# Optimization experiments

Hardware: AMD Instinct MI355X
Metric: run time of the kernel (lower is better)

Reference implementation:

```python
import jax, jax.numpy as jnp
import numpy as np

V, E, H = 32000, 512, 512
B, T = 4, 2048


def setup_inputs() -> dict:
    key = jax.random.key(0)
    ks = jax.random.split(key, 10)
    s_e = 1.0 / np.sqrt(E)
    s_h = 1.0 / np.sqrt(H)
    emb = jax.random.normal(ks[0], (V, E), jnp.float32) * 0.02
    emb = emb.at[0].set(0.0)  # padding_idx=0
    return {
        "x": jax.random.randint(ks[1], (B, T), 0, V),
        "emb": emb,
        "W_ih": jax.random.uniform(ks[2], (3 * H, E), jnp.float32, -s_h, s_h),
        "W_hh": jax.random.uniform(ks[3], (3 * H, H), jnp.float32, -s_h, s_h),
        "b_ih": jnp.zeros((3 * H,), jnp.float32),
        "b_hh": jnp.zeros((3 * H,), jnp.float32),
        "Wq": jax.random.uniform(ks[4], (H, H), jnp.float32, -s_h, s_h),
        "bq": jnp.zeros((H,), jnp.float32),
        "Wk": jax.random.uniform(ks[5], (H, H), jnp.float32, -s_h, s_h),
        "bk": jnp.zeros((H,), jnp.float32),
        "Wv": jax.random.uniform(ks[6], (H, H), jnp.float32, -s_h, s_h),
        "bv": jnp.zeros((H,), jnp.float32),
        "Wfc": jax.random.uniform(ks[7], (V, H), jnp.float32, -s_h, s_h),
        "bfc": jnp.zeros((V,), jnp.float32),
    }


def _gru(z, W_ih, W_hh, b_ih, b_hh):
    # z: [B,T,E] -> hidden states [B,T,H]; PyTorch gate order r,z,n.
    b, t, _ = z.shape
    h_dim = W_hh.shape[1]
    xg = jnp.einsum('bte,ge->btg', z, W_ih) + b_ih  # [B,T,3H]

    def step(h, xt):
        gh = h @ W_hh.T + b_hh
        xr, xz, xn = jnp.split(xt, 3, axis=-1)
        hr, hz, hn = jnp.split(gh, 3, axis=-1)
        r = jax.nn.sigmoid(xr + hr)
        zg = jax.nn.sigmoid(xz + hz)
        n = jnp.tanh(xn + r * hn)
        h_new = (1.0 - zg) * n + zg * h
        return h_new, h_new

    h0 = jnp.zeros((b, h_dim), z.dtype)
    _, hs = jax.lax.scan(step, h0, jnp.swapaxes(xg, 0, 1))  # [T,B,H]
    return jnp.swapaxes(hs, 0, 1)


def reference(x, emb, W_ih, W_hh, b_ih, b_hh, Wq, bq, Wk, bk, Wv, bv, Wfc, bfc):
    z = emb[x]                                   # [B,T,E]
    h = _gru(z, W_ih, W_hh, b_ih, b_hh)          # [B,T,H]
    q = h @ Wq.T + bq
    k = h @ Wk.T + bk
    v = h @ Wv.T + bv
    hd = h.shape[-1]
    score = jnp.einsum('bqd,bkd->bqk', q, k) / jnp.sqrt(jnp.float32(hd))
    t = score.shape[-1]
    causal = jnp.triu(jnp.ones((t, t), bool), k=1)  # True above diagonal
    score = jnp.where(causal[None], jnp.float32(-1e9), score)
    attn = jax.nn.softmax(score, axis=-1)
    ctx = jnp.einsum('bqk,bkd->bqd', attn, v)
    return ctx @ Wfc.T + bfc                      # [B,T,V]
```

## Files before the change

### kernel.cpp

```cpp
#include <hip/hip_runtime.h>

#define Bn 4
#define Tn 2048
#define Hn 512
#define En 512
#define Vn 32000
#define G3 1536
#define BT (Bn*Tn)

typedef __bf16 bf16x8 __attribute__((ext_vector_type(8)));
typedef float f32x4 __attribute__((ext_vector_type(4)));

__device__ __forceinline__ unsigned short f2bf(float f) {
  unsigned int u = __float_as_uint(f);
  u += 0x7fffu + ((u >> 16) & 1u);
  return (unsigned short)(u >> 16);
}

__global__ __launch_bounds__(256) void cvt_bf16_kernel(const float* __restrict__ in,
                                                       unsigned short* __restrict__ outp) {
  size_t idx = (size_t)blockIdx.x * 256 + threadIdx.x;
  float4 f = *(const float4*)(in + idx * 4);
  uint2 o;
  o.x = (unsigned int)f2bf(f.x) | ((unsigned int)f2bf(f.y) << 16);
  o.y = (unsigned int)f2bf(f.z) | ((unsigned int)f2bf(f.w) << 16);
  *(uint2*)(outp + idx * 4) = o;
}

__global__ __launch_bounds__(256) void gather_emb_kernel(const int* __restrict__ x,
                                                         const float* __restrict__ emb,
                                                         unsigned short* __restrict__ embb) {
  size_t idx = ((size_t)blockIdx.x * 256 + threadIdx.x) * 8;
  int row = (int)(idx >> 9), e = (int)(idx & 511);
  const float* src = emb + (size_t)x[row] * En + e;
  float4 f0 = *(const float4*)(src);
  float4 f1 = *(const float4*)(src + 4);
  uint4 o;
  o.x = (unsigned)f2bf(f0.x) | ((unsigned)f2bf(f0.y) << 16);
  o.y = (unsigned)f2bf(f0.z) | ((unsigned)f2bf(f0.w) << 16);
  o.z = (unsigned)f2bf(f1.x) | ((unsigned)f2bf(f1.y) << 16);
  o.w = (unsigned)f2bf(f1.z) | ((unsigned)f2bf(f1.w) << 16);
  *(uint4*)(embb + idx) = o;
}

__global__ __launch_bounds__(256) void xg_mm_kernel(const unsigned short* __restrict__ A,
                                                    const unsigned short* __restrict__ Bw,
                                                    const float* __restrict__ bias,
                                                    float* __restrict__ out) {
  __shared__ unsigned short a_lds[128 * 40];
  __shared__ unsigned short b_lds[128 * 40];
  int n0 = blockIdx.x * 128, m0 = blockIdx.y * 128;
  int tid = threadIdx.x;
  int wid = tid >> 6, lane = tid & 63;
  int wm = wid >> 1, wn = wid & 1;
  f32x4 acc[4][4];
#pragma unroll
  for (int mf = 0; mf < 4; ++mf)
#pragma unroll
    for (int nf = 0; nf < 4; ++nf) {
      acc[mf][nf][0] = 0.0f; acc[mf][nf][1] = 0.0f;
      acc[mf][nf][2] = 0.0f; acc[mf][nf][3] = 0.0f;
    }
  int kcol = (lane >> 4) * 8;
  int rbase = lane & 15;
  for (int k0 = 0; k0 < 512; k0 += 32) {
#pragma unroll
    for (int sidx = 0; sidx < 2; ++sidx) {
      int slot = tid + sidx * 256;
      int row = slot >> 2, c8 = (slot & 3) * 8;
      uint4 av = *(const uint4*)(A  + (size_t)(m0 + row) * 512 + k0 + c8);
      *(uint4*)&a_lds[row * 40 + c8] = av;
      uint4 bv = *(const uint4*)(Bw + (size_t)(n0 + row) * 512 + k0 + c8);
      *(uint4*)&b_lds[row * 40 + c8] = bv;
    }
    __syncthreads();
    bf16x8 af[4], bf[4];
#pragma unroll
    for (int mf = 0; mf < 4; ++mf)
      af[mf] = *(const bf16x8*)&a_lds[(wm*64 + mf*16 + rbase) * 40 + kcol];
#pragma unroll
    for (int nf = 0; nf < 4; ++nf)
      bf[nf] = *(const bf16x8*)&b_lds[(wn*64 + nf*16 + rbase) * 40 + kcol];
#pragma unroll
    for (int mf = 0; mf < 4; ++mf)
#pragma unroll
      for (int nf = 0; nf < 4; ++nf)
        acc[mf][nf] = __builtin_amdgcn_mfma_f32_16x16x32_bf16(af[mf], bf[nf], acc[mf][nf], 0, 0, 0);
    __syncthreads();
  }
  int rgrp = (lane >> 4) * 4;
#pragma unroll
  for (int mf = 0; mf < 4; ++mf)
#pragma unroll
    for (int nf = 0; nf < 4; ++nf) {
      int col = n0 + wn*64 + nf*16 + (lane & 15);
      float bc = bias[col];
#pragma unroll
      for (int i2 = 0; i2 < 4; ++i2) {
        int row = m0 + wm*64 + mf*16 + rgrp + i2;
        out[(size_t)row * G3 + col] = acc[mf][nf][i2] + bc;
      }
    }
}

__global__ __launch_bounds__(256) void qkv_mm_kernel(const unsigned short* __restrict__ A,
                                                     const unsigned short* __restrict__ Bw,
                                                     const float* __restrict__ bq,
                                                     const float* __restrict__ bk,
                                                     const float* __restrict__ bv,
                                                     unsigned short* __restrict__ qb,
                                                     unsigned short* __restrict__ kb,
                                                     unsigned short* __restrict__ vb) {
  __shared__ unsigned short a_lds[128 * 40];
  __shared__ unsigned short b_lds[128 * 40];
  int n0 = blockIdx.x * 128, m0 = blockIdx.y * 128;
  int seg = n0 >> 9;
  const float* bias = (seg == 0) ? bq : (seg == 1) ? bk : bv;
  unsigned short* outp = (seg == 0) ? qb : (seg == 1) ? kb : vb;
  int nc0 = n0 & 511;
  int tid = threadIdx.x;
  int wid = tid >> 6, lane = tid & 63;
  int wm = wid >> 1, wn = wid & 1;
  f32x4 acc[4][4];
#pragma unroll
  for (int mf = 0; mf < 4; ++mf)
#pragma unroll
    for (int nf = 0; nf < 4; ++nf) {
      acc[mf][nf][0] = 0.0f; acc[mf][nf][1] = 0.0f;
      acc[mf][nf][2] = 0.0f; acc[mf][nf][3] = 0.0f;
    }
  int kcol = (lane >> 4) * 8;
  int rbase = lane & 15;
  for (int k0 = 0; k0 < 512; k0 += 32) {
#pragma unroll
    for (int sidx = 0; sidx < 2; ++sidx) {
      int slot = tid + sidx * 256;
      int row = slot >> 2, c8 = (slot & 3) * 8;
      uint4 av = *(const uint4*)(A  + (size_t)(m0 + row) * 512 + k0 + c8);
      *(uint4*)&a_lds[row * 40 + c8] = av;
      uint4 bv4 = *(const uint4*)(Bw + (size_t)(n0 + row) * 512 + k0 + c8);
      *(uint4*)&b_lds[row * 40 + c8] = bv4;
    }
    __syncthreads();
    bf16x8 af[4], bf[4];
#pragma unroll
    for (int mf = 0; mf < 4; ++mf)
      af[mf] = *(const bf16x8*)&a_lds[(wm*64 + mf*16 + rbase) * 40 + kcol];
#pragma unroll
    for (int nf = 0; nf < 4; ++nf)
      bf[nf] = *(const bf16x8*)&b_lds[(wn*64 + nf*16 + rbase) * 40 + kcol];
#pragma unroll
    for (int mf = 0; mf < 4; ++mf)
#pragma unroll
      for (int nf = 0; nf < 4; ++nf)
        acc[mf][nf] = __builtin_amdgcn_mfma_f32_16x16x32_bf16(af[mf], bf[nf], acc[mf][nf], 0, 0, 0);
    __syncthreads();
  }
  int rgrp = (lane >> 4) * 4;
#pragma unroll
  for (int mf = 0; mf < 4; ++mf)
#pragma unroll
    for (int nf = 0; nf < 4; ++nf) {
      int col = nc0 + wn*64 + nf*16 + (lane & 15);
      float bc = bias[col];
#pragma unroll
      for (int i2 = 0; i2 < 4; ++i2) {
        int row = m0 + wm*64 + mf*16 + rgrp + i2;
        outp[(size_t)row * Hn + col] = f2bf(acc[mf][nf][i2] + bc);
      }
    }
}

__global__ __launch_bounds__(256, 1) void gru_kernel(const float* __restrict__ Whh,
                                                     const float* __restrict__ bhh,
                                                     const float* __restrict__ xg,
                                                     unsigned short* __restrict__ hsb,
                                                     unsigned long long* __restrict__ th) {
  __shared__ float w_lds[6][512];
  int tid = threadIdx.x;
  int g = blockIdx.x;
  int jb = g * 2;
  int w = tid >> 6, lane = tid & 63;

  for (int d = 0; d < 6; ++d) {
    const float* wr = Whh + (size_t)((d >> 1) * 512 + jb + (d & 1)) * 512;
    int e0 = tid, e1 = tid + 256;
    int s0 = e0 >> 6, l0 = e0 & 63;
    int s1 = e1 >> 6, l1 = e1 & 63;
    w_lds[d][e0] = wr[(s0 >> 1) * 128 + 2 * l0 + (s0 & 1)];
    w_lds[d][e1] = wr[(s1 >> 1) * 128 + 2 * l1 + (s1 & 1)];
  }
  float bh_r = 0.0f, bh_z = 0.0f, bh_n = 0.0f;
  if (lane < 2) {
    bh_r = bhh[jb + lane];
    bh_z = bhh[512 + jb + lane];
    bh_n = bhh[1024 + jb + lane];
  }
  float hown = 0.0f;
  __syncthreads();

  const unsigned long long RDYM = 0x0000000100000001ULL;
  for (int t = 0; t < Tn; ++t) {
    float xr = 0.0f, xz = 0.0f, xn = 0.0f;
    if (lane < 2) {
      size_t xb = ((size_t)(w * Tn + t)) * G3 + jb + lane;
      xr = xg[xb]; xz = xg[xb + 512]; xn = xg[xb + 1024];
    }
    float hlo[4], hhi[4];
    if (t > 0) {
      const unsigned long long* tp = th + (size_t)(t - 1) * 1024 + w * 256;
      unsigned long long v[4];
      unsigned rdy = 0;
      do {
#pragma unroll
        for (int q = 0; q < 4; ++q)
          if (!(rdy & (1u << q)))
            v[q] = __hip_atomic_load(tp + q * 64 + lane, __ATOMIC_RELAXED,
                                     __HIP_MEMORY_SCOPE_AGENT);
#pragma unroll
        for (int q = 0; q < 4; ++q)
          if ((v[q] & RDYM) == RDYM) rdy |= 1u << q;
      } while (!__all(rdy == 15u));
#pragma unroll
      for (int q = 0; q < 4; ++q) {
        hlo[q] = __uint_as_float((unsigned)v[q]);
        hhi[q] = __uint_as_float((unsigned)(v[q] >> 32));
      }
    } else {
#pragma unroll
      for (int q = 0; q < 4; ++q) { hlo[q] = 0.0f; hhi[q] = 0.0f; }
    }

    float p[6];
#pragma unroll
    for (int d = 0; d < 6; ++d) {
      float s = w_lds[d][lane] * hlo[0];
      s = fmaf(w_lds[d][64 + lane], hhi[0], s);
#pragma unroll
      for (int q = 1; q < 4; ++q) {
        s = fmaf(w_lds[d][(2 * q) * 64 + lane], hlo[q], s);
        s = fmaf(w_lds[d][(2 * q + 1) * 64 + lane], hhi[q], s);
      }
      p[d] = s;
    }

    float mm[3];
#pragma unroll
    for (int j = 0; j < 3; ++j) {
      float a = p[2 * j], b = p[2 * j + 1];
      bool odd = (lane & 1);
      float send = odd ? a : b;
      float rx = __shfl_xor(send, 1);
      float m = (odd ? b : a) + rx;
      m += __shfl_xor(m, 2);
      m += __shfl_xor(m, 4);
      m += __shfl_xor(m, 8);
      m += __shfl_xor(m, 16);
      m += __shfl_xor(m, 32);
      mm[j] = m;
    }
    if (lane < 2) {
      float dr = mm[0], dz = mm[1], dn = mm[2];
      float rr = __builtin_amdgcn_rcpf(1.0f + __expf(-(xr + dr + bh_r)));
      float zz = __builtin_amdgcn_rcpf(1.0f + __expf(-(xz + dz + bh_z)));
      float ta = xn + rr * (dn + bh_n);
      float nn = 1.0f - 2.0f * __builtin_amdgcn_rcpf(__expf(2.0f * ta) + 1.0f);
      hown = (1.0f - zz) * nn + zz * hown;
    }
    unsigned myb = __float_as_uint(hown) | 1u;
    unsigned other = __shfl(myb, 1);
    if (lane == 0) {
      unsigned long long pk = ((unsigned long long)other << 32) | myb;
      __hip_atomic_store(th + (size_t)t * 1024 + w * 256 + g, pk,
                         __ATOMIC_RELAXED, __HIP_MEMORY_SCOPE_AGENT);
    }
    if (lane < 2)
      hsb[((size_t)w * Tn + t) * Hn + jb + lane] = f2bf(hown);
  }
}

__global__ __launch_bounds__(256) void vt_kernel(const unsigned short* __restrict__ v,
                                                 unsigned short* __restrict__ vT) {
  __shared__ unsigned short tl[64][80];
  int b = blockIdx.z;
  int t0 = blockIdx.x * 64, e0 = blockIdx.y * 64;
  int tid = threadIdx.x;
  int r = tid >> 2, c16 = (tid & 3) * 16;
  const unsigned short* src = v + (size_t)b * Tn * Hn + (size_t)(t0 + r) * Hn + e0 + c16;
  uint4 a0 = *(const uint4*)(src);
  uint4 a1 = *(const uint4*)(src + 8);
  *(uint4*)&tl[r][c16]     = a0;
  *(uint4*)&tl[r][c16 + 8] = a1;
  __syncthreads();
  unsigned short* dst = vT + (size_t)b * Hn * Tn + (size_t)(e0 + r) * Tn + t0 + c16;
  unsigned int o[8];
#pragma unroll
  for (int ii = 0; ii < 8; ++ii)
    o[ii] = (unsigned)tl[c16 + 2*ii][r] | ((unsigned)tl[c16 + 2*ii + 1][r] << 16);
  uint4 o0; o0.x = o[0]; o0.y = o[1]; o0.z = o[2]; o0.w = o[3];
  uint4 o1; o1.x = o[4]; o1.y = o[5]; o1.z = o[6]; o1.w = o[7];
  *(uint4*)(dst)     = o0;
  *(uint4*)(dst + 8) = o1;
}

__global__ __launch_bounds__(256) void score_kernel(const unsigned short* __restrict__ qb,
                                                    const unsigned short* __restrict__ kbp,
                                                    float* __restrict__ s) {
  if (blockIdx.x > blockIdx.y) return;
  __shared__ unsigned short a_lds[128 * 40];
  __shared__ unsigned short b_lds[128 * 40];
  int b = blockIdx.z;
  int n0 = blockIdx.x * 128, m0 = blockIdx.y * 128;
  const unsigned short* A  = qb  + (size_t)b * Tn * Hn;
  const unsigned short* Bw = kbp + (size_t)b * Tn * Hn;
  int tid = threadIdx.x;
  int wid = tid >> 6, lane = tid & 63;
  int wm = wid >> 1, wn = wid & 1;
  f32x4 acc[4][4];
#pragma unroll
  for (int mf = 0; mf < 4; ++mf)
#pragma unroll
    for (int nf = 0; nf < 4; ++nf) {
      acc[mf][nf][0] = 0.0f; acc[mf][nf][1] = 0.0f;
      acc[mf][nf][2] = 0.0f; acc[mf][nf][3] = 0.0f;
    }
  int kcol = (lane >> 4) * 8;
  int rbase = lane & 15;
  for (int k0 = 0; k0 < Hn; k0 += 32) {
#pragma unroll
    for (int sidx = 0; sidx < 2; ++sidx) {
      int slot = tid + sidx * 256;
      int row = slot >> 2, c8 = (slot & 3) * 8;
      uint4 av = *(const uint4*)(A  + (size_t)(m0 + row) * Hn + k0 + c8);
      *(uint4*)&a_lds[row * 40 + c8] = av;
      uint4 bv = *(const uint4*)(Bw + (size_t)(n0 + row) * Hn + k0 + c8);
      *(uint4*)&b_lds[row * 40 + c8] = bv;
    }
    __syncthreads();
    bf16x8 af[4], bf[4];
#pragma unroll
    for (int mf = 0; mf < 4; ++mf)
      af[mf] = *(const bf16x8*)&a_lds[(wm*64 + mf*16 + rbase) * 40 + kcol];
#pragma unroll
    for (int nf = 0; nf < 4; ++nf)
      bf[nf] = *(const bf16x8*)&b_lds[(wn*64 + nf*16 + rbase) * 40 + kcol];
#pragma unroll
    for (int mf = 0; mf < 4; ++mf)
#pragma unroll
      for (int nf = 0; nf < 4; ++nf)
        acc[mf][nf] = __builtin_amdgcn_mfma_f32_16x16x32_bf16(af[mf], bf[nf], acc[mf][nf], 0, 0, 0);
    __syncthreads();
  }
  const float scale = 0.04419417382415922f;
  int rgrp = (lane >> 4) * 4;
#pragma unroll
  for (int mf = 0; mf < 4; ++mf)
#pragma unroll
    for (int nf = 0; nf < 4; ++nf) {
      int col = n0 + wn*64 + nf*16 + (lane & 15);
#pragma unroll
      for (int i2 = 0; i2 < 4; ++i2) {
        int row = m0 + wm*64 + mf*16 + rgrp + i2;
        s[(size_t)b*Tn*Tn + (size_t)row*Tn + col] = acc[mf][nf][i2] * scale;
      }
    }
}

__global__ __launch_bounds__(256) void softmax_kernel(float* __restrict__ s,
                                                      unsigned short* __restrict__ ab) {
  int row = blockIdx.x;
  int b = row >> 11, i = row & 2047;
  float* p = s + (size_t)b*Tn*Tn + (size_t)i*Tn;
  unsigned short* a = ab + ((size_t)b*Tn + i) * Tn;
  int len = i + 1;
  int padEnd = ((i >> 7) + 1) << 7;
  int tid = threadIdx.x;
  __shared__ float redm[4];
  __shared__ float reds[4];
  float m = -1e30f;
  for (int j = tid; j < len; j += 256) m = fmaxf(m, p[j]);
#pragma unroll
  for (int off = 32; off > 0; off >>= 1) m = fmaxf(m, __shfl_down(m, off));
  if ((tid & 63) == 0) redm[tid >> 6] = m;
  __syncthreads();
  if (tid == 0) redm[0] = fmaxf(fmaxf(redm[0], redm[1]), fmaxf(redm[2], redm[3]));
  __syncthreads();
  m = redm[0];
  float sum = 0.0f;
  for (int j = tid; j < len; j += 256) {
    float e = __expf(p[j] - m);
    p[j] = e;
    sum += e;
  }
#pragma unroll
  for (int off = 32; off > 0; off >>= 1) sum += __shfl_down(sum, off);
  if ((tid & 63) == 0) reds[tid >> 6] = sum;
  __syncthreads();
  if (tid == 0) reds[0] = reds[0] + reds[1] + reds[2] + reds[3];
  __syncthreads();
  float inv = 1.0f / reds[0];
  for (int j = tid; j < len; j += 256) a[j] = f2bf(p[j] * inv);
  for (int j = len + tid; j < padEnd; j += 256) a[j] = 0;
}

__global__ __launch_bounds__(256) void ctx_kernel(const unsigned short* __restrict__ ab,
                                                  const unsigned short* __restrict__ vT,
                                                  unsigned short* __restrict__ ctxb) {
  __shared__ unsigned short a_lds[128 * 40];
  __shared__ unsigned short b_lds[128 * 40];
  int b = blockIdx.z;
  int n0 = blockIdx.x * 128, m0 = blockIdx.y * 128;
  int kmax = (blockIdx.y + 1) * 128;
  const unsigned short* A  = ab + (size_t)b * Tn * Tn;
  const unsigned short* Bw = vT + (size_t)b * Hn * Tn;
  int tid = threadIdx.x;
  int wid = tid >> 6, lane = tid & 63;
  int wm = wid >> 1, wn = wid & 1;
  f32x4 acc[4][4];
#pragma unroll
  for (int mf = 0; mf < 4; ++mf)
#pragma unroll
    for (int nf = 0; nf < 4; ++nf) {
      acc[mf][nf][0] = 0.0f; acc[mf][nf][1] = 0.0f;
      acc[mf][nf][2] = 0.0f; acc[mf][nf][3] = 0.0f;
    }
  int kcol = (lane >> 4) * 8;
  int rbase = lane & 15;
  for (int k0 = 0; k0 < kmax; k0 += 32) {
#pragma unroll
    for (int sidx = 0; sidx < 2; ++sidx) {
      int slot = tid + sidx * 256;
      int row = slot >> 2, c8 = (slot & 3) * 8;
      uint4 av = *(const uint4*)(A  + (size_t)(m0 + row) * Tn + k0 + c8);
      *(uint4*)&a_lds[row * 40 + c8] = av;
      uint4 bv = *(const uint4*)(Bw + (size_t)(n0 + row) * Tn + k0 + c8);
      *(uint4*)&b_lds[row * 40 + c8] = bv;
    }
    __syncthreads();
    bf16x8 af[4], bf[4];
#pragma unroll
    for (int mf = 0; mf < 4; ++mf)
      af[mf] = *(const bf16x8*)&a_lds[(wm*64 + mf*16 + rbase) * 40 + kcol];
#pragma unroll
    for (int nf = 0; nf < 4; ++nf)
      bf[nf] = *(const bf16x8*)&b_lds[(wn*64 + nf*16 + rbase) * 40 + kcol];
#pragma unroll
    for (int mf = 0; mf < 4; ++mf)
#pragma unroll
      for (int nf = 0; nf < 4; ++nf)
        acc[mf][nf] = __builtin_amdgcn_mfma_f32_16x16x32_bf16(af[mf], bf[nf], acc[mf][nf], 0, 0, 0);
    __syncthreads();
  }
  int rgrp = (lane >> 4) * 4;
#pragma unroll
  for (int mf = 0; mf < 4; ++mf)
#pragma unroll
    for (int nf = 0; nf < 4; ++nf) {
      int col = n0 + wn*64 + nf*16 + (lane & 15);
#pragma unroll
      for (int i2 = 0; i2 < 4; ++i2) {
        int row = m0 + wm*64 + mf*16 + rgrp + i2;
        ctxb[((size_t)b*Tn + row) * Hn + col] = f2bf(acc[mf][nf][i2]);
      }
    }
}

__global__ __launch_bounds__(256) void logits_kernel(const unsigned short* __restrict__ A,
                                                     const unsigned short* __restrict__ Bw,
                                                     const float* __restrict__ bias,
                                                     float* __restrict__ out) {
  __shared__ unsigned short a_lds[128 * 40];
  __shared__ unsigned short b_lds[128 * 40];
  int n0 = blockIdx.x * 128, m0 = blockIdx.y * 128;
  int tid = threadIdx.x;
  int wid = tid >> 6, lane = tid & 63;
  int wm = wid >> 1, wn = wid & 1;
  f32x4 acc[4][4];
#pragma unroll
  for (int mf = 0; mf < 4; ++mf)
#pragma unroll
    for (int nf = 0; nf < 4; ++nf) {
      acc[mf][nf][0] = 0.0f; acc[mf][nf][1] = 0.0f;
      acc[mf][nf][2] = 0.0f; acc[mf][nf][3] = 0.0f;
    }
  int kcol = (lane >> 4) * 8;
  int rbase = lane & 15;
  for (int k0 = 0; k0 < 512; k0 += 32) {
#pragma unroll
    for (int sidx = 0; sidx < 2; ++sidx) {
      int slot = tid + sidx * 256;
      int row = slot >> 2, c8 = (slot & 3) * 8;
      uint4 av = *(const uint4*)(A  + (size_t)(m0 + row) * 512 + k0 + c8);
      *(uint4*)&a_lds[row * 40 + c8] = av;
      uint4 bv = *(const uint4*)(Bw + (size_t)(n0 + row) * 512 + k0 + c8);
      *(uint4*)&b_lds[row * 40 + c8] = bv;
    }
    __syncthreads();
    bf16x8 af[4], bf[4];
#pragma unroll
    for (int mf = 0; mf < 4; ++mf)
      af[mf] = *(const bf16x8*)&a_lds[(wm*64 + mf*16 + rbase) * 40 + kcol];
#pragma unroll
    for (int nf = 0; nf < 4; ++nf)
      bf[nf] = *(const bf16x8*)&b_lds[(wn*64 + nf*16 + rbase) * 40 + kcol];
#pragma unroll
    for (int mf = 0; mf < 4; ++mf)
#pragma unroll
      for (int nf = 0; nf < 4; ++nf)
        acc[mf][nf] = __builtin_amdgcn_mfma_f32_16x16x32_bf16(af[mf], bf[nf], acc[mf][nf], 0, 0, 0);
    __syncthreads();
  }
  int rgrp = (lane >> 4) * 4;
#pragma unroll
  for (int mf = 0; mf < 4; ++mf)
#pragma unroll
    for (int nf = 0; nf < 4; ++nf) {
      int col = n0 + wn*64 + nf*16 + (lane & 15);
      float bc = bias[col];
#pragma unroll
      for (int i2 = 0; i2 < 4; ++i2) {
        int row = m0 + wm*64 + mf*16 + rgrp + i2;
        out[(size_t)row * Vn + col] = acc[mf][nf][i2] + bc;
      }
    }
}

extern "C" void kernel_launch(void* const* d_in, const int* in_sizes, int n_in,
                              void* d_out, int out_size, void* d_ws, size_t ws_size,
                              hipStream_t stream) {
  const int*   x   = (const int*)d_in[0];
  const float* emb = (const float*)d_in[1];
  const float* Wih = (const float*)d_in[2];
  const float* Whh = (const float*)d_in[3];
  const float* bih = (const float*)d_in[4];
  const float* bhh = (const float*)d_in[5];
  const float* Wq  = (const float*)d_in[6];
  const float* bq  = (const float*)d_in[7];
  const float* Wk  = (const float*)d_in[8];
  const float* bk  = (const float*)d_in[9];
  const float* Wv  = (const float*)d_in[10];
  const float* bv  = (const float*)d_in[11];
  const float* Wfc = (const float*)d_in[12];
  const float* bfc = (const float*)d_in[13];
  float* out = (float*)d_out;

  char* ws = (char*)d_ws;
  unsigned short* hsb   = (unsigned short*)(ws);
  unsigned short* qb    = (unsigned short*)(ws + 8388608);
  unsigned short* kb    = (unsigned short*)(ws + 16777216);
  unsigned short* vb    = (unsigned short*)(ws + 25165824);
  unsigned short* vTb   = (unsigned short*)(ws + 33554432);
  unsigned short* ctxb  = (unsigned short*)(ws + 41943040);
  unsigned short* wfcb  = (unsigned short*)(ws + 50331648);
  unsigned short* embb  = (unsigned short*)(ws + 83886080);
  unsigned short* wihb  = (unsigned short*)(ws + 92274688);
  unsigned short* wqkvb = (unsigned short*)(ws + 93847552);

  float* scores = out;
  float* xg = (float*)((char*)d_out + 67108864);
  unsigned long long* th = (unsigned long long*)((char*)d_out + 117440512);
  unsigned short* attnb  = (unsigned short*)((char*)d_out + 150994944);

  hipMemsetAsync(th, 0, (size_t)Tn * 1024 * 8, stream);
  cvt_bf16_kernel<<<16000, 256, 0, stream>>>(Wfc, wfcb);
  cvt_bf16_kernel<<<768, 256, 0, stream>>>(Wih, wihb);
  cvt_bf16_kernel<<<256, 256, 0, stream>>>(Wq, wqkvb);
  cvt_bf16_kernel<<<256, 256, 0, stream>>>(Wk, wqkvb + 262144);
  cvt_bf16_kernel<<<256, 256, 0, stream>>>(Wv, wqkvb + 524288);
  gather_emb_kernel<<<2048, 256, 0, stream>>>(x, emb, embb);
  xg_mm_kernel<<<dim3(12, 64), 256, 0, stream>>>(embb, wihb, bih, xg);
  gru_kernel<<<256, 256, 0, stream>>>(Whh, bhh, xg, hsb, th);
  qkv_mm_kernel<<<dim3(12, 64), 256, 0, stream>>>(hsb, wqkvb, bq, bk, bv, qb, kb, vb);
  vt_kernel<<<dim3(32, 8, Bn), 256, 0, stream>>>(vb, vTb);
  score_kernel<<<dim3(16, 16, Bn), 256, 0, stream>>>(qb, kb, scores);
  softmax_kernel<<<BT, 256, 0, stream>>>(scores, attnb);
  ctx_kernel<<<dim3(4, 16, Bn), 256, 0, stream>>>(attnb, vTb, ctxb);
  logits_kernel<<<dim3(250, 64), 256, 0, stream>>>(ctxb, wfcb, bfc, out);
}
```

Baseline: 4.546 ms.

## Merge prep kernels and pipeline GRU step polling with double-buffered loads

Folds the five bf16 conversion launches and the embedding gather into a single prep kernel so fewer launches are issued. In the GRU recurrence, the spin-wait on the previous step's hidden state now keeps two sets of atomic loads in flight alternately, to cut the latency of each polling round. Each of the two owning lanes now writes its own 32-bit flagged value directly, which removes a shuffle and the 64-bit packed store. This relies on each 32-bit half carrying its own ready bit, which the existing mask check already tests.

```diff
diff --git a/kernel.cpp b/kernel.cpp
--- a/kernel.cpp
+++ b/kernel.cpp
@@ -17,30 +17,51 @@
   return (unsigned short)(u >> 16);
 }
 
-__global__ __launch_bounds__(256) void cvt_bf16_kernel(const float* __restrict__ in,
-                                                       unsigned short* __restrict__ outp) {
-  size_t idx = (size_t)blockIdx.x * 256 + threadIdx.x;
+__device__ __forceinline__ void cvt4(const float* __restrict__ in,
+                                     unsigned short* __restrict__ outp, size_t idx) {
   float4 f = *(const float4*)(in + idx * 4);
   uint2 o;
-  o.x = (unsigned int)f2bf(f.x) | ((unsigned int)f2bf(f.y) << 16);
-  o.y = (unsigned int)f2bf(f.z) | ((unsigned int)f2bf(f.w) << 16);
+  o.x = (unsigned)f2bf(f.x) | ((unsigned)f2bf(f.y) << 16);
+  o.y = (unsigned)f2bf(f.z) | ((unsigned)f2bf(f.w) << 16);
   *(uint2*)(outp + idx * 4) = o;
 }
 
-__global__ __launch_bounds__(256) void gather_emb_kernel(const int* __restrict__ x,
-                                                         const float* __restrict__ emb,
-                                                         unsigned short* __restrict__ embb) {
-  size_t idx = ((size_t)blockIdx.x * 256 + threadIdx.x) * 8;
-  int row = (int)(idx >> 9), e = (int)(idx & 511);
-  const float* src = emb + (size_t)x[row] * En + e;
-  float4 f0 = *(const float4*)(src);
-  float4 f1 = *(const float4*)(src + 4);
-  uint4 o;
-  o.x = (unsigned)f2bf(f0.x) | ((unsigned)f2bf(f0.y) << 16);
-  o.y = (unsigned)f2bf(f0.z) | ((unsigned)f2bf(f0.w) << 16);
-  o.z = (unsigned)f2bf(f1.x) | ((unsigned)f2bf(f1.y) << 16);
-  o.w = (unsigned)f2bf(f1.z) | ((unsigned)f2bf(f1.w) << 16);
-  *(uint4*)(embb + idx) = o;
+__global__ __launch_bounds__(256) void prep_kernel(const float* __restrict__ Wfc,
+                                                   unsigned short* __restrict__ wfcb,
+                                                   const float* __restrict__ Wih,
+                                                   unsigned short* __restrict__ wihb,
+                                                   const float* __restrict__ Wq,
+                                                   const float* __restrict__ Wk,
+                                                   const float* __restrict__ Wv,
+                                                   unsigned short* __restrict__ wqkvb,
+                                                   const int* __restrict__ x,
+                                                   const float* __restrict__ emb,
+                                                   unsigned short* __restrict__ embb) {
+  int b = blockIdx.x;
+  int tid = threadIdx.x;
+  if (b < 16000) {
+    cvt4(Wfc, wfcb, (size_t)b * 256 + tid);
+  } else if (b < 16768) {
+    cvt4(Wih, wihb, (size_t)(b - 16000) * 256 + tid);
+  } else if (b < 17024) {
+    cvt4(Wq, wqkvb, (size_t)(b - 16768) * 256 + tid);
+  } else if (b < 17280) {
+    cvt4(Wk, wqkvb + 262144, (size_t)(b - 17024) * 256 + tid);
+  } else if (b < 17536) {
+    cvt4(Wv, wqkvb + 524288, (size_t)(b - 17280) * 256 + tid);
+  } else {
+    size_t idx = ((size_t)(b - 17536) * 256 + tid) * 8;
+    int row = (int)(idx >> 9), e = (int)(idx & 511);
+    const float* src = emb + (size_t)x[row] * En + e;
+    float4 f0 = *(const float4*)(src);
+    float4 f1 = *(const float4*)(src + 4);
+    uint4 o;
+    o.x = (unsigned)f2bf(f0.x) | ((unsigned)f2bf(f0.y) << 16);
+    o.y = (unsigned)f2bf(f0.z) | ((unsigned)f2bf(f0.w) << 16);
+    o.z = (unsigned)f2bf(f1.x) | ((unsigned)f2bf(f1.y) << 16);
+    o.w = (unsigned)f2bf(f1.z) | ((unsigned)f2bf(f1.w) << 16);
+    *(uint4*)(embb + idx) = o;
+  }
 }
 
 __global__ __launch_bounds__(256) void xg_mm_kernel(const unsigned short* __restrict__ A,
@@ -197,6 +218,7 @@
     bh_n = bhh[1024 + jb + lane];
   }
   float hown = 0.0f;
+  unsigned* th32 = (unsigned*)th;
   __syncthreads();
 
   const unsigned long long RDYM = 0x0000000100000001ULL;
@@ -209,18 +231,40 @@
     float hlo[4], hhi[4];
     if (t > 0) {
       const unsigned long long* tp = th + (size_t)(t - 1) * 1024 + w * 256;
-      unsigned long long v[4];
+      unsigned long long A[4], B[4], v[4];
       unsigned rdy = 0;
-      do {
+#pragma unroll
+      for (int q = 0; q < 4; ++q)
+        A[q] = __hip_atomic_load(tp + q * 64 + lane, __ATOMIC_RELAXED,
+                                 __HIP_MEMORY_SCOPE_AGENT);
+#pragma unroll
+      for (int q = 0; q < 4; ++q)
+        B[q] = __hip_atomic_load(tp + q * 64 + lane, __ATOMIC_RELAXED,
+                                 __HIP_MEMORY_SCOPE_AGENT);
+      for (;;) {
+#pragma unroll
+        for (int q = 0; q < 4; ++q)
+          if (!(rdy & (1u << q)) && ((A[q] & RDYM) == RDYM)) {
+            v[q] = A[q]; rdy |= 1u << q;
+          }
+        if (__all(rdy == 15u)) break;
 #pragma unroll
         for (int q = 0; q < 4; ++q)
           if (!(rdy & (1u << q)))
-            v[q] = __hip_atomic_load(tp + q * 64 + lane, __ATOMIC_RELAXED,
+            A[q] = __hip_atomic_load(tp + q * 64 + lane, __ATOMIC_RELAXED,
                                      __HIP_MEMORY_SCOPE_AGENT);
 #pragma unroll
         for (int q = 0; q < 4; ++q)
-          if ((v[q] & RDYM) == RDYM) rdy |= 1u << q;
-      } while (!__all(rdy == 15u));
+          if (!(rdy & (1u << q)) && ((B[q] & RDYM) == RDYM)) {
+            v[q] = B[q]; rdy |= 1u << q;
+          }
+        if (__all(rdy == 15u)) break;
+#pragma unroll
+        for (int q = 0; q < 4; ++q)
+          if (!(rdy & (1u << q)))
+            B[q] = __hip_atomic_load(tp + q * 64 + lane, __ATOMIC_RELAXED,
+                                     __HIP_MEMORY_SCOPE_AGENT);
+      }
 #pragma unroll
       for (int q = 0; q < 4; ++q) {
         hlo[q] = __uint_as_float((unsigned)v[q]);
@@ -266,16 +310,11 @@
       float ta = xn + rr * (dn + bh_n);
       float nn = 1.0f - 2.0f * __builtin_amdgcn_rcpf(__expf(2.0f * ta) + 1.0f);
       hown = (1.0f - zz) * nn + zz * hown;
-    }
-    unsigned myb = __float_as_uint(hown) | 1u;
-    unsigned other = __shfl(myb, 1);
-    if (lane == 0) {
-      unsigned long long pk = ((unsigned long long)other << 32) | myb;
-      __hip_atomic_store(th + (size_t)t * 1024 + w * 256 + g, pk,
+      unsigned myb = __float_as_uint(hown) | 1u;
+      __hip_atomic_store(th32 + (size_t)t * 2048 + (w * 256 + g) * 2 + lane, myb,
                          __ATOMIC_RELAXED, __HIP_MEMORY_SCOPE_AGENT);
-    }
-    if (lane < 2)
       hsb[((size_t)w * Tn + t) * Hn + jb + lane] = f2bf(hown);
+    }
   }
 }
 
@@ -562,12 +601,8 @@
   unsigned short* attnb  = (unsigned short*)((char*)d_out + 150994944);
 
   hipMemsetAsync(th, 0, (size_t)Tn * 1024 * 8, stream);
-  cvt_bf16_kernel<<<16000, 256, 0, stream>>>(Wfc, wfcb);
-  cvt_bf16_kernel<<<768, 256, 0, stream>>>(Wih, wihb);
-  cvt_bf16_kernel<<<256, 256, 0, stream>>>(Wq, wqkvb);
-  cvt_bf16_kernel<<<256, 256, 0, stream>>>(Wk, wqkvb + 262144);
-  cvt_bf16_kernel<<<256, 256, 0, stream>>>(Wv, wqkvb + 524288);
-  gather_emb_kernel<<<2048, 256, 0, stream>>>(x, emb, embb);
+  prep_kernel<<<19584, 256, 0, stream>>>(Wfc, wfcb, Wih, wihb, Wq, Wk, Wv,
+                                         wqkvb, x, emb, embb);
   xg_mm_kernel<<<dim3(12, 64), 256, 0, stream>>>(embb, wihb, bih, xg);
   gru_kernel<<<256, 256, 0, stream>>>(Whh, bhh, xg, hsb, th);
   qkv_mm_kernel<<<dim3(12, 64), 256, 0, stream>>>(hsb, wqkvb, bq, bk, bv, qb, kb, vb);
```

Result: slower. 13.00 ms (+186.0%).
